# Kernel tuning notes

Hardware: AMD Instinct MI355X
Metric: run time of the kernel (lower is better)

## Reference

```python
import jax, jax.numpy as jnp
import numpy as np

P, N, M = 4, 8192, 8192

def setup_inputs() -> dict:
    key = jax.random.key(0)
    k1, k2, k3, k4, k5 = jax.random.split(key, 5)
    return {
        "camera_pts": jax.random.normal(k1, (P, N, 3), dtype=jnp.float32),
        "cad_pts": jax.random.normal(k2, (P, M, 3), dtype=jnp.float32),
        "part_weight": jax.random.uniform(k3, (P,), dtype=jnp.float32),
        "rot_quat": jax.random.normal(k4, (P, 4), dtype=jnp.float32),
        "tra": jax.random.normal(k5, (P, 3, 1), dtype=jnp.float32),
    }

def _quat_to_rot(q):
    # q: [P,4] in (w,x,y,z) order, normalized outside
    a, b, c, d = q[:, 0], q[:, 1], q[:, 2], q[:, 3]
    rows = jnp.stack([
        1 - 2*c*c - 2*d*d, 2*b*c - 2*a*d,     2*a*c + 2*b*d,
        2*b*c + 2*a*d,     1 - 2*b*b - 2*d*d, 2*c*d - 2*a*b,
        2*b*d - 2*a*c,     2*a*b + 2*c*d,     1 - 2*b*b - 2*c*c,
    ], axis=-1)  # [P,9]
    return rows.reshape(-1, 3, 3)

def _chamfer(x, y):
    # x: [N,4], y: [M,4] -> scalar bidirectional chamfer (Euclidean, not squared)
    x2 = jnp.sum(x * x, axis=-1)              # [N]
    y2 = jnp.sum(y * y, axis=-1)              # [M]
    d2 = x2[:, None] + y2[None, :] - 2.0 * (x @ y.T)
    dist = jnp.sqrt(jnp.clip(d2, 0.0))        # [N,M]
    return jnp.mean(jnp.min(dist, axis=1)) + jnp.mean(jnp.min(dist, axis=0))

def reference(camera_pts, cad_pts, part_weight, rot_quat, tra):
    q = rot_quat / jnp.linalg.norm(rot_quat, axis=1, keepdims=True)
    rot = _quat_to_rot(q)                                       # [P,3,3]
    top = jnp.concatenate([rot, tra], axis=2)                   # [P,3,4]
    bottom = jnp.broadcast_to(jnp.array([[[0.0, 0.0, 0.0, 1.0]]], dtype=rot.dtype), (rot.shape[0], 1, 4))
    transforms = jnp.concatenate([top, bottom], axis=1)         # [P,4,4]
    ones_cad = jnp.ones(cad_pts.shape[:-1] + (1,), dtype=cad_pts.dtype)
    ones_cam = jnp.ones(camera_pts.shape[:-1] + (1,), dtype=camera_pts.dtype)
    cad_h = jnp.concatenate([cad_pts, ones_cad], axis=-1)       # [P,M,4]
    cam_h = jnp.concatenate([camera_pts, ones_cam], axis=-1)    # [P,N,4]
    cad_base = jnp.einsum('pij,pmj->pmi', transforms, cad_h)    # [P,M,4]
    cd = jax.vmap(_chamfer)(cad_base, cam_h)                    # [P]
    all_objective = jnp.sum(part_weight * cd)
    return all_objective, jax.lax.stop_gradient(transforms)
```

## Files before the change

### kernel.cpp

```cpp
#include <hip/hip_runtime.h>
#include <math.h>

#define NP 4
#define NN 8192
#define NM 8192

#define PK_A_F4 0
#define PK_B_F4 (NP * NM)
#define MINS_OFF ((NP * NM + NP * NN) * 4)
#define MINB_REL (NP * NM)

#define TQ 8
#define QT 2048
#define SPLITS 32
#define SPAN 256

#define RED_BLOCKS 128

__device__ inline float min3f(float a, float b, float c) {
    float d;
    asm("v_min3_f32 %0, %1, %2, %3" : "=v"(d) : "v"(a), "v"(b), "v"(c));
    return d;
}

__device__ inline void make_transform(const float* __restrict__ quat,
                                      const float* __restrict__ tra,
                                      int p, float T[12]) {
    float q0 = quat[p * 4 + 0], q1 = quat[p * 4 + 1];
    float q2 = quat[p * 4 + 2], q3 = quat[p * 4 + 3];
    float inv = 1.0f / sqrtf(q0 * q0 + q1 * q1 + q2 * q2 + q3 * q3);
    float a = q0 * inv, b = q1 * inv, c = q2 * inv, d = q3 * inv;
    T[0] = 1.0f - 2.0f * c * c - 2.0f * d * d;
    T[1] = 2.0f * b * c - 2.0f * a * d;
    T[2] = 2.0f * a * c + 2.0f * b * d;
    T[3] = tra[p * 3 + 0];
    T[4] = 2.0f * b * c + 2.0f * a * d;
    T[5] = 1.0f - 2.0f * b * b - 2.0f * d * d;
    T[6] = 2.0f * c * d - 2.0f * a * b;
    T[7] = tra[p * 3 + 1];
    T[8] = 2.0f * b * d - 2.0f * a * c;
    T[9] = 2.0f * a * b + 2.0f * c * d;
    T[10] = 1.0f - 2.0f * b * b - 2.0f * c * c;
    T[11] = tra[p * 3 + 2];
}

__global__ __launch_bounds__(256) void prep_kernel(
    const float* __restrict__ cam, const float* __restrict__ cad,
    const float* __restrict__ quat, const float* __restrict__ tra,
    float* __restrict__ ws, float* __restrict__ out) {
    int idx = blockIdx.x * 256 + threadIdx.x;
    const float INF = __uint_as_float(0x7f800000u);

    if (idx < NP * NM) {
        int p = idx >> 13;
        int m = idx & (NM - 1);
        float T[12];
        make_transform(quat, tra, p, T);
        float x = cad[(p * NM + m) * 3 + 0];
        float y = cad[(p * NM + m) * 3 + 1];
        float z = cad[(p * NM + m) * 3 + 2];
        float vx = fmaf(T[0], x, fmaf(T[1], y, fmaf(T[2], z, T[3])));
        float vy = fmaf(T[4], x, fmaf(T[5], y, fmaf(T[6], z, T[7])));
        float vz = fmaf(T[8], x, fmaf(T[9], y, fmaf(T[10], z, T[11])));
        float h = 0.5f * (vx * vx + vy * vy + vz * vz);
        ((float4*)ws)[PK_A_F4 + idx] = make_float4(vx, vy, vz, h);
        ws[MINS_OFF + idx] = INF;
    } else {
        int k = idx - NP * NM;
        float vx = cam[k * 3 + 0];
        float vy = cam[k * 3 + 1];
        float vz = cam[k * 3 + 2];
        float h = 0.5f * (vx * vx + vy * vy + vz * vz);
        ((float4*)ws)[PK_B_F4 + k] = make_float4(vx, vy, vz, h);
        ws[MINS_OFF + MINB_REL + k] = INF;
    }

    if (idx < 64) {
        int p2 = idx >> 4;
        int r = (idx >> 2) & 3;
        int c = idx & 3;
        float T[12];
        make_transform(quat, tra, p2, T);
        float v;
        if (r == 3)
            v = (c == 3) ? 1.0f : 0.0f;
        else
            v = T[r * 4 + c];
        out[1 + idx] = v;
    } else if (idx == 64) {
        out[0] = 0.0f;
    }
}

__global__ __launch_bounds__(256) void chamfer_kernel(
    const float4* __restrict__ packed, float* __restrict__ mins) {
    int tid = threadIdx.x;
    int p = blockIdx.z >> 1;
    int role = blockIdx.z & 1;

    const float4* Q;
    const float4* T;
    float* minarr;
    if (role == 0) {
        Q = packed + PK_A_F4 + p * NM;
        T = packed + PK_B_F4 + p * NN;
        minarr = mins + p * NM;
    } else {
        Q = packed + PK_B_F4 + p * NN;
        T = packed + PK_A_F4 + p * NM;
        minarr = mins + MINB_REL + p * NN;
    }

    const float INF = __uint_as_float(0x7f800000u);
    int q0 = blockIdx.x * QT + tid;
    float qx[TQ], qy[TQ], qz[TQ], qw[TQ], tmin[TQ];
#pragma unroll
    for (int k = 0; k < TQ; ++k) {
        float4 v = Q[q0 + k * 256];
        qx[k] = v.x; qy[k] = v.y; qz[k] = v.z; qw[k] = v.w;
        tmin[k] = INF;
    }

    int tbase = blockIdx.y * SPAN;
#pragma unroll 4
    for (int j = 0; j < SPAN; j += 2) {
        float4 t0 = T[tbase + j];
        float4 t1 = T[tbase + j + 1];
#pragma unroll
        for (int k = 0; k < TQ; ++k) {
            float s0 = fmaf(-qx[k], t0.x, fmaf(-qy[k], t0.y, fmaf(-qz[k], t0.z, t0.w)));
            float s1 = fmaf(-qx[k], t1.x, fmaf(-qy[k], t1.y, fmaf(-qz[k], t1.z, t1.w)));
            tmin[k] = min3f(tmin[k], s0, s1);
        }
    }

#pragma unroll
    for (int k = 0; k < TQ; ++k) {
        float d2 = 2.0f * (qw[k] + tmin[k]);
        d2 = fmaxf(d2, 0.0f);
        atomicMin((unsigned int*)&minarr[q0 + k * 256], __float_as_uint(d2));
    }
}

__global__ __launch_bounds__(256) void finalize_kernel(
    const float* __restrict__ ws, const float* __restrict__ w,
    float* __restrict__ out) {
    const float* vals = ws + MINS_OFF;
    int i = blockIdx.x * 256 + threadIdx.x;
    int tid = threadIdx.x;

    float wl[4] = {w[0], w[1], w[2], w[3]};

    int i2 = i + 32768;
    float acc = wl[(i >> 13) & 3] * sqrtf(vals[i]) +
                wl[(i2 >> 13) & 3] * sqrtf(vals[i2]);

#pragma unroll
    for (int off = 32; off > 0; off >>= 1) acc += __shfl_down(acc, off, 64);

    __shared__ float wsum[4];
    if ((tid & 63) == 0) wsum[tid >> 6] = acc;
    __syncthreads();
    if (tid == 0) {
        float blocksum = (wsum[0] + wsum[1] + wsum[2] + wsum[3]) * (1.0f / 8192.0f);
        atomicAdd(out, blocksum);
    }
}

extern "C" void kernel_launch(void* const* d_in, const int* in_sizes, int n_in,
                              void* d_out, int out_size, void* d_ws, size_t ws_size,
                              hipStream_t stream) {
    const float* cam = (const float*)d_in[0];
    const float* cad = (const float*)d_in[1];
    const float* w = (const float*)d_in[2];
    const float* quat = (const float*)d_in[3];
    const float* tra = (const float*)d_in[4];
    float* out = (float*)d_out;
    float* ws = (float*)d_ws;

    prep_kernel<<<(NP * (NM + NN)) / 256, 256, 0, stream>>>(cam, cad, quat, tra, ws, out);

    dim3 grid(NM / QT, SPLITS, 2 * NP);
    chamfer_kernel<<<grid, 256, 0, stream>>>((const float4*)ws, ws + MINS_OFF);

    finalize_kernel<<<RED_BLOCKS, 256, 0, stream>>>(ws, w, out);
}
```

Measured before the change: 127.6 us.

## Use packed FMA with wave-uniform query broadcast and partial-min buffers instead of atomics

Restructures the chamfer kernel so each lane keeps 8 target points in registers and loops over a chunk of query points read as wave-uniform duplicated pairs. The inner product is evaluated with v_pk_fma_f32 on two targets at once. Per-split partial minima go to a buffer and are reduced in finalize, replacing the atomicMin scatter and the INF initialisation. This aims to halve the FMA instruction count and remove atomics. In exchange the min operations are no longer fused into min3, there are more partial writes, and the finalize kernel does more reads.

```diff
diff --git a/kernel.cpp b/kernel.cpp
--- a/kernel.cpp
+++ b/kernel.cpp
@@ -5,21 +5,21 @@
 #define NN 8192
 #define NM 8192
 
-#define PK_A_F4 0
-#define PK_B_F4 (NP * NM)
-#define MINS_OFF ((NP * NM + NP * NN) * 4)
-#define MINB_REL (NP * NM)
+#define QA_OFF 0
+#define QB_OFF 262144
+#define TA_OFF 524288
+#define TB_OFF 655360
+#define PART_OFF 786432
 
-#define TQ 8
-#define QT 2048
-#define SPLITS 32
-#define SPAN 256
+#define TT 8
+#define QSPLIT 16
+#define QCHUNK 512
 
-#define RED_BLOCKS 128
+typedef float float2v __attribute__((ext_vector_type(2)));
 
-__device__ inline float min3f(float a, float b, float c) {
-    float d;
-    asm("v_min3_f32 %0, %1, %2, %3" : "=v"(d) : "v"(a), "v"(b), "v"(c));
+__device__ inline float2v pk_fma(float2v a, float2v b, float2v c) {
+    float2v d;
+    asm("v_pk_fma_f32 %0, %1, %2, %3" : "=v"(d) : "v"(a), "v"(b), "v"(c));
     return d;
 }
 
@@ -49,31 +49,34 @@
     const float* __restrict__ quat, const float* __restrict__ tra,
     float* __restrict__ ws, float* __restrict__ out) {
     int idx = blockIdx.x * 256 + threadIdx.x;
-    const float INF = __uint_as_float(0x7f800000u);
 
+    float vx, vy, vz;
+    int qoff, toff, local;
     if (idx < NP * NM) {
         int p = idx >> 13;
-        int m = idx & (NM - 1);
         float T[12];
         make_transform(quat, tra, p, T);
-        float x = cad[(p * NM + m) * 3 + 0];
-        float y = cad[(p * NM + m) * 3 + 1];
-        float z = cad[(p * NM + m) * 3 + 2];
-        float vx = fmaf(T[0], x, fmaf(T[1], y, fmaf(T[2], z, T[3])));
-        float vy = fmaf(T[4], x, fmaf(T[5], y, fmaf(T[6], z, T[7])));
-        float vz = fmaf(T[8], x, fmaf(T[9], y, fmaf(T[10], z, T[11])));
-        float h = 0.5f * (vx * vx + vy * vy + vz * vz);
-        ((float4*)ws)[PK_A_F4 + idx] = make_float4(vx, vy, vz, h);
-        ws[MINS_OFF + idx] = INF;
+        float x = cad[idx * 3 + 0];
+        float y = cad[idx * 3 + 1];
+        float z = cad[idx * 3 + 2];
+        vx = fmaf(T[0], x, fmaf(T[1], y, fmaf(T[2], z, T[3])));
+        vy = fmaf(T[4], x, fmaf(T[5], y, fmaf(T[6], z, T[7])));
+        vz = fmaf(T[8], x, fmaf(T[9], y, fmaf(T[10], z, T[11])));
+        qoff = QA_OFF; toff = TA_OFF; local = idx;
     } else {
-        int k = idx - NP * NM;
-        float vx = cam[k * 3 + 0];
-        float vy = cam[k * 3 + 1];
-        float vz = cam[k * 3 + 2];
-        float h = 0.5f * (vx * vx + vy * vy + vz * vz);
-        ((float4*)ws)[PK_B_F4 + k] = make_float4(vx, vy, vz, h);
-        ws[MINS_OFF + MINB_REL + k] = INF;
+        local = idx - NP * NM;
+        vx = cam[local * 3 + 0];
+        vy = cam[local * 3 + 1];
+        vz = cam[local * 3 + 2];
+        qoff = QB_OFF; toff = TB_OFF;
     }
+    float h = 0.5f * (vx * vx + vy * vy + vz * vz);
+    float* q = ws + qoff + (size_t)local * 8;
+    q[0] = -vx; q[1] = -vx;
+    q[2] = -vy; q[3] = -vy;
+    q[4] = -vz; q[5] = -vz;
+    q[6] = h;   q[7] = h;
+    ((float4*)(ws + toff))[local] = make_float4(vx, vy, vz, h);
 
     if (idx < 64) {
         int p2 = idx >> 4;
@@ -93,67 +96,73 @@
 }
 
 __global__ __launch_bounds__(256) void chamfer_kernel(
-    const float4* __restrict__ packed, float* __restrict__ mins) {
+    const float* __restrict__ ws, float* __restrict__ part) {
     int tid = threadIdx.x;
+    int lane = tid & 63;
+    int w = tid >> 6;
+    int dir = blockIdx.z & 1;
     int p = blockIdx.z >> 1;
-    int role = blockIdx.z & 1;
+    int qs = blockIdx.y;
+    int slab = blockIdx.x * 4 + w;
+    const float INF = __uint_as_float(0x7f800000u);
 
-    const float4* Q;
-    const float4* T;
-    float* minarr;
-    if (role == 0) {
-        Q = packed + PK_A_F4 + p * NM;
-        T = packed + PK_B_F4 + p * NN;
-        minarr = mins + p * NM;
-    } else {
-        Q = packed + PK_B_F4 + p * NN;
-        T = packed + PK_A_F4 + p * NM;
-        minarr = mins + MINB_REL + p * NN;
+    const float4* T = (const float4*)(ws + (dir == 0 ? TA_OFF : TB_OFF)) + p * 8192;
+    const float2v* Q = (const float2v*)(ws + (dir == 0 ? QB_OFF : QA_OFF)) + (size_t)p * 8192 * 4;
+
+    int tbase = slab * 512;
+    float2v TX[TT / 2], TY[TT / 2], TZ[TT / 2], TH[TT / 2], mB[TT / 2];
+#pragma unroll
+    for (int j = 0; j < TT; ++j) {
+        float4 t = T[tbase + j * 64 + lane];
+        TX[j >> 1][j & 1] = t.x;
+        TY[j >> 1][j & 1] = t.y;
+        TZ[j >> 1][j & 1] = t.z;
+        TH[j >> 1][j & 1] = t.w;
+        mB[j >> 1][j & 1] = INF;
     }
 
-    const float INF = __uint_as_float(0x7f800000u);
-    int q0 = blockIdx.x * QT + tid;
-    float qx[TQ], qy[TQ], qz[TQ], qw[TQ], tmin[TQ];
+    const float2v* qp = Q + (size_t)(qs * QCHUNK) * 4;
+#pragma unroll 4
+    for (int qi = 0; qi < QCHUNK; ++qi) {
+        float2v sX = qp[qi * 4 + 0];
+        float2v sY = qp[qi * 4 + 1];
+        float2v sZ = qp[qi * 4 + 2];
+        float2v sH = qp[qi * 4 + 3];
 #pragma unroll
-    for (int k = 0; k < TQ; ++k) {
-        float4 v = Q[q0 + k * 256];
-        qx[k] = v.x; qy[k] = v.y; qz[k] = v.z; qw[k] = v.w;
-        tmin[k] = INF;
-    }
-
-    int tbase = blockIdx.y * SPAN;
-#pragma unroll 4
-    for (int j = 0; j < SPAN; j += 2) {
-        float4 t0 = T[tbase + j];
-        float4 t1 = T[tbase + j + 1];
-#pragma unroll
-        for (int k = 0; k < TQ; ++k) {
-            float s0 = fmaf(-qx[k], t0.x, fmaf(-qy[k], t0.y, fmaf(-qz[k], t0.z, t0.w)));
-            float s1 = fmaf(-qx[k], t1.x, fmaf(-qy[k], t1.y, fmaf(-qz[k], t1.z, t1.w)));
-            tmin[k] = min3f(tmin[k], s0, s1);
+        for (int i = 0; i < TT / 2; ++i) {
+            float2v u = pk_fma(TZ[i], sZ, sH);
+            u = pk_fma(TY[i], sY, u);
+            u = pk_fma(TX[i], sX, u);
+            mB[i][0] = fminf(mB[i][0], u[0]);
+            mB[i][1] = fminf(mB[i][1], u[1]);
         }
     }
 
+    float* dst = part + ((size_t)dir * QSPLIT + qs) * 32768 + p * 8192;
 #pragma unroll
-    for (int k = 0; k < TQ; ++k) {
-        float d2 = 2.0f * (qw[k] + tmin[k]);
-        d2 = fmaxf(d2, 0.0f);
-        atomicMin((unsigned int*)&minarr[q0 + k * 256], __float_as_uint(d2));
+    for (int j = 0; j < TT; ++j) {
+        dst[tbase + j * 64 + lane] = mB[j >> 1][j & 1] + TH[j >> 1][j & 1];
     }
 }
 
 __global__ __launch_bounds__(256) void finalize_kernel(
     const float* __restrict__ ws, const float* __restrict__ w,
     float* __restrict__ out) {
-    const float* vals = ws + MINS_OFF;
+    const float* part = ws + PART_OFF;
     int i = blockIdx.x * 256 + threadIdx.x;
     int tid = threadIdx.x;
+    const float INF = __uint_as_float(0x7f800000u);
 
-    float wl[4] = {w[0], w[1], w[2], w[3]};
+    float va = INF, vb = INF;
+#pragma unroll 8
+    for (int s = 0; s < QSPLIT; ++s) {
+        va = fminf(va, part[(size_t)s * 32768 + i]);
+        vb = fminf(vb, part[((size_t)QSPLIT + s) * 32768 + i]);
+    }
 
-    int i2 = i + 32768;
-    float acc = wl[(i >> 13) & 3] * sqrtf(vals[i]) +
-                wl[(i2 >> 13) & 3] * sqrtf(vals[i2]);
+    float wp = w[(i >> 13) & 3];
+    float acc = wp * (sqrtf(fmaxf(2.0f * va, 0.0f)) +
+                      sqrtf(fmaxf(2.0f * vb, 0.0f)));
 
 #pragma unroll
     for (int off = 32; off > 0; off >>= 1) acc += __shfl_down(acc, off, 64);
@@ -178,10 +187,10 @@
     float* out = (float*)d_out;
     float* ws = (float*)d_ws;
 
-    prep_kernel<<<(NP * (NM + NN)) / 256, 256, 0, stream>>>(cam, cad, quat, tra, ws, out);
+    prep_kernel<<<256, 256, 0, stream>>>(cam, cad, quat, tra, ws, out);
 
-    dim3 grid(NM / QT, SPLITS, 2 * NP);
-    chamfer_kernel<<<grid, 256, 0, stream>>>((const float4*)ws, ws + MINS_OFF);
+    dim3 grid(4, QSPLIT, 2 * NP);
+    chamfer_kernel<<<grid, 256, 0, stream>>>(ws, ws + PART_OFF);
 
-    finalize_kernel<<<RED_BLOCKS, 256, 0, stream>>>(ws, w, out);
+    finalize_kernel<<<128, 256, 0, stream>>>(ws, w, out);
 }
```

Measured after the change: 159.9 us. 25.4% more time.
